# Kernel optimization log

Hardware: AMD Instinct MI355X
Metric: run time of the kernel (lower is better)

## Reference

```python
import jax, jax.numpy as jnp
import numpy as np
import math

B, N, F_IN, F_OUT = 8, 2048, 128, 128


def _uniform(key, shape, stdv):
    return jax.random.uniform(key, shape, dtype=jnp.float32, minval=-stdv, maxval=stdv)


def setup_inputs() -> dict:
    key = jax.random.key(0)
    k_x, k_a, k_w, k_att, k_bw, k_ba = jax.random.split(key, 6)
    X = jax.random.normal(k_x, (B, N, F_IN), dtype=jnp.float32)
    # dense 0/1 adjacency, as consumed by torch.bmm(A, ...)
    A = jax.random.randint(k_a, (B, N, N), 0, 2).astype(jnp.float32)
    stdv_W = 1.0 / math.sqrt(F_OUT)        # W.size(1) == n_fea_out
    stdv_a = 1.0 / math.sqrt(2 * F_OUT)    # a.size(1) == 2*n_fea_out
    W = _uniform(k_w, (F_IN, F_OUT), stdv_W)
    a = _uniform(k_att, (1, 2 * F_OUT), stdv_a)
    bias_W = _uniform(k_bw, (F_OUT,), stdv_W)
    bias_a = _uniform(k_ba, (N,), stdv_a)
    return {"X": X, "A": A, "W": W, "a": a, "bias_a": bias_a, "bias_W": bias_W}


def reference(X, A, W, a, bias_a, bias_W):
    # XW: [B, N, F_out]
    XW = jnp.einsum('bnf,fo->bno', X, W)
    f = W.shape[1]
    # Original materializes Z[b,i,j] = concat(XW[b,j], XW[b,i]) then dots with a.
    # This is separable: Z1[b,i,j] = a[:f]@XW[b,j] + a[f:]@XW[b,i] + bias_a[j]
    a_j = a[0, :f]   # multiplies XW[b, j]
    a_i = a[0, f:]   # multiplies XW[b, i]
    s_j = jnp.einsum('bnf,f->bn', XW, a_j)  # [B, N]
    s_i = jnp.einsum('bnf,f->bn', XW, a_i)  # [B, N]
    Z1 = s_i[:, :, None] + s_j[:, None, :] + bias_a[None, None, :]  # [B, N, N]
    den = jnp.exp(Z1)
    num = jnp.einsum('bik,bkj->bij', A, den)  # torch.bmm(A, denominator)
    # where numerator == 0 the torch code leaves att uninitialized; use 0 deterministically
    nz = num != 0
    att = jnp.where(nz, den / jnp.where(nz, num, 1.0), 0.0)
    buf = jnp.einsum('bij,bjf->bif', att, XW)
    H = jnp.einsum('bij,bjf->bif', A, buf) + bias_W
    return H
```

## Files before the change

kernel.cpp:

```cpp
#include <hip/hip_runtime.h>

#define BB 8
#define NN 2048
#define FF 128


__global__ __launch_bounds__(128) void k0_wai(const float* __restrict__ W,
                                              const float* __restrict__ a,
                                              float* __restrict__ w_ai) {
    int c = threadIdx.x;
    float s = 0.f;
#pragma unroll 8
    for (int f = 0; f < FF; ++f) s += W[c * FF + f] * a[FF + f];
    w_ai[c] = s;
}

__global__ __launch_bounds__(256) void k1_p_xsum(const float* __restrict__ X,
                                                 const float* __restrict__ w_ai,
                                                 float* __restrict__ p,
                                                 float* __restrict__ xsum) {
    __shared__ float xls[FF];
    int gr0 = blockIdx.x * 32;
    int b = gr0 >> 11;
    int lane = threadIdx.x & 63;
    int wave = threadIdx.x >> 6;
    int half = lane >> 5;
    int l32 = lane & 31;

    if (threadIdx.x < FF) xls[threadIdx.x] = 0.f;
    __syncthreads();

    float4 wv = ((const float4*)w_ai)[l32];
    float4 cs = make_float4(0.f, 0.f, 0.f, 0.f);
    const float4* X4 = (const float4*)(X + (size_t)gr0 * FF);

#pragma unroll
    for (int it = 0; it < 4; ++it) {
        int rloc = wave * 8 + it * 2 + half;
        float4 xv = X4[(size_t)rloc * 32 + l32];
        cs.x += xv.x; cs.y += xv.y; cs.z += xv.z; cs.w += xv.w;
        float s = xv.x * wv.x + xv.y * wv.y + xv.z * wv.z + xv.w * wv.w;
#pragma unroll
        for (int off = 16; off; off >>= 1) s += __shfl_xor(s, off, 64);
        if (l32 == 0) p[(size_t)gr0 + rloc] = expf(s);
    }

    atomicAdd(&xls[l32 * 4 + 0], cs.x);
    atomicAdd(&xls[l32 * 4 + 1], cs.y);
    atomicAdd(&xls[l32 * 4 + 2], cs.z);
    atomicAdd(&xls[l32 * 4 + 3], cs.w);
    __syncthreads();
    if (threadIdx.x < FF) atomicAdd(&xsum[b * FF + threadIdx.x], xls[threadIdx.x]);
}

__global__ __launch_bounds__(128) void k2_S(const float* __restrict__ W,
                                            const float* __restrict__ xsum,
                                            float* __restrict__ S) {
    int b = blockIdx.x;
    int f = threadIdx.x;
    float s = 0.f;
#pragma unroll 8
    for (int c = 0; c < FF; ++c) s += xsum[b * FF + c] * W[c * FF + f];
    S[b * FF + f] = s;
}

__global__ __launch_bounds__(256) void k3_r(const float* __restrict__ A,
                                            const float* __restrict__ p,
                                            float* __restrict__ r,
                                            unsigned long long* __restrict__ pk) {
    __shared__ float p_lds[NN];
    int row0 = blockIdx.x * 8;
    int b = row0 >> 11;

    const float4* p4 = (const float4*)(p + (size_t)b * NN);
    float4* pl4 = (float4*)p_lds;
    pl4[threadIdx.x]       = p4[threadIdx.x];
    pl4[threadIdx.x + 256] = p4[threadIdx.x + 256];
    __syncthreads();

    int lane = threadIdx.x & 63;
    int wave = threadIdx.x >> 6;
    int rowA = row0 + wave * 2;
    int rowB = rowA + 1;
    const float4* Aa = (const float4*)(A + (size_t)rowA * NN);
    const float4* Ab = (const float4*)(A + (size_t)rowB * NN);

    int c = lane & 3;
    float accA = 0.f, accB = 0.f;
#pragma unroll
    for (int it = 0; it < 8; ++it) {
        float4 pv = pl4[it * 64 + lane];
        float4 va = Aa[it * 64 + lane];
        float4 vb = Ab[it * 64 + lane];
        accA += va.x * pv.x + va.y * pv.y + va.z * pv.z + va.w * pv.w;
        accB += vb.x * pv.x + vb.y * pv.y + vb.z * pv.z + vb.w * pv.w;

        unsigned long long a0 = __ballot(va.x != 0.f);
        unsigned long long a1 = __ballot(va.y != 0.f);
        unsigned long long a2 = __ballot(va.z != 0.f);
        unsigned long long a3 = __ballot(va.w != 0.f);
        unsigned long long b0 = __ballot(vb.x != 0.f);
        unsigned long long b1 = __ballot(vb.y != 0.f);
        unsigned long long b2 = __ballot(vb.z != 0.f);
        unsigned long long b3 = __ballot(vb.w != 0.f);
        if (lane < 8) {
            unsigned long long alo = (c & 1) ? a1 : a0;
            unsigned long long ahi = (c & 1) ? a3 : a2;
            unsigned long long am  = (c & 2) ? ahi : alo;
            unsigned long long blo = (c & 1) ? b1 : b0;
            unsigned long long bhi = (c & 1) ? b3 : b2;
            unsigned long long bm  = (c & 2) ? bhi : blo;
            int row = (lane < 4) ? rowA : rowB;
            unsigned long long m = (lane < 4) ? am : bm;
            pk[(size_t)row * 32 + it * 4 + c] = m;
        }
    }
#pragma unroll
    for (int off = 32; off; off >>= 1) {
        accA += __shfl_xor(accA, off, 64);
        accB += __shfl_xor(accB, off, 64);
    }

    if (lane == 0) {
        r[rowA] = (accA != 0.f) ? (p_lds[rowA & (NN - 1)] / accA) : 0.f;
        r[rowB] = (accB != 0.f) ? (p_lds[rowB & (NN - 1)] / accB) : 0.f;
    }
}

__global__ __launch_bounds__(256) void k4_H(const unsigned long long* __restrict__ pk,
                                            const float* __restrict__ rr,
                                            const float* __restrict__ S,
                                            const float* __restrict__ bias_W,
                                            float* __restrict__ Hout) {
    __shared__ float r_lds[NN];
    __shared__ float s_lds[FF];
    __shared__ float bw_lds[FF];
    int row0 = blockIdx.x * 8;
    int b = row0 >> 11;

    const float4* r4 = (const float4*)(rr + (size_t)b * NN);
    float4* rl4 = (float4*)r_lds;
    rl4[threadIdx.x]       = r4[threadIdx.x];
    rl4[threadIdx.x + 256] = r4[threadIdx.x + 256];
    if (threadIdx.x < FF) {
        s_lds[threadIdx.x]  = S[b * FF + threadIdx.x];
        bw_lds[threadIdx.x] = bias_W[threadIdx.x];
    }
    __syncthreads();

    int lane = threadIdx.x & 63;
    int wave = threadIdx.x >> 6;
    int rowA = row0 + wave * 2;
    int rowB = rowA + 1;

    unsigned long long w =
        pk[(size_t)(lane < 32 ? rowA : rowB) * 32 + (lane & 31)];

    float accA = 0.f, accB = 0.f;
#pragma unroll
    for (int it = 0; it < 8; ++it) {
        float4 rv = rl4[it * 64 + lane];
        unsigned long long mA0 = __shfl(w, it * 4 + 0, 64);
        unsigned long long mA1 = __shfl(w, it * 4 + 1, 64);
        unsigned long long mA2 = __shfl(w, it * 4 + 2, 64);
        unsigned long long mA3 = __shfl(w, it * 4 + 3, 64);
        unsigned long long mB0 = __shfl(w, 32 + it * 4 + 0, 64);
        unsigned long long mB1 = __shfl(w, 32 + it * 4 + 1, 64);
        unsigned long long mB2 = __shfl(w, 32 + it * 4 + 2, 64);
        unsigned long long mB3 = __shfl(w, 32 + it * 4 + 3, 64);
        if ((mA0 >> lane) & 1ull) accA += rv.x;
        if ((mA1 >> lane) & 1ull) accA += rv.y;
        if ((mA2 >> lane) & 1ull) accA += rv.z;
        if ((mA3 >> lane) & 1ull) accA += rv.w;
        if ((mB0 >> lane) & 1ull) accB += rv.x;
        if ((mB1 >> lane) & 1ull) accB += rv.y;
        if ((mB2 >> lane) & 1ull) accB += rv.z;
        if ((mB3 >> lane) & 1ull) accB += rv.w;
    }
#pragma unroll
    for (int off = 32; off; off >>= 1) {
        accA += __shfl_xor(accA, off, 64);
        accB += __shfl_xor(accB, off, 64);
    }

    float2 sv = ((const float2*)s_lds)[lane];
    float2 bv = ((const float2*)bw_lds)[lane];
    float2* H2 = (float2*)Hout;
    float2 ha, hb;
    ha.x = accA * sv.x + bv.x;  ha.y = accA * sv.y + bv.y;
    hb.x = accB * sv.x + bv.x;  hb.y = accB * sv.y + bv.y;
    H2[(size_t)rowA * 64 + lane] = ha;
    H2[(size_t)rowB * 64 + lane] = hb;
}

extern "C" void kernel_launch(void* const* d_in, const int* in_sizes, int n_in,
                              void* d_out, int out_size, void* d_ws, size_t ws_size,
                              hipStream_t stream) {
    const float* X      = (const float*)d_in[0];
    const float* A      = (const float*)d_in[1];
    const float* W      = (const float*)d_in[2];
    const float* a      = (const float*)d_in[3];
    const float* bias_W = (const float*)d_in[5];
    float* out = (float*)d_out;

    float* ws   = (float*)d_ws;
    float* w_ai = ws;
    float* xsum = ws + 128;
    float* S    = ws + 1152;
    float* p    = ws + 2176;
    float* r    = ws + 18560;
    unsigned long long* pk = (unsigned long long*)(ws + 34944);

    hipMemsetAsync(xsum, 0, BB * FF * sizeof(float), stream);

    k0_wai<<<1, 128, 0, stream>>>(W, a, w_ai);
    k1_p_xsum<<<(BB * NN) / 32, 256, 0, stream>>>(X, w_ai, p, xsum);
    k2_S<<<BB, 128, 0, stream>>>(W, xsum, S);
    k3_r<<<(BB * NN) / 8, 256, 0, stream>>>(A, p, r, pk);
    k4_H<<<(BB * NN) / 8, 256, 0, stream>>>(pk, r, S, bias_W, out);
}
```

Measured before the change: 240.7 us.

## Fold tiny prologue kernels into main kernels and drop memset

Computes W·a_i redundantly in every k1 block instead of a separate launch. k1 now writes per-block partial column sums instead of using global atomics, and an extra block 0 in k3 reduces them and computes S. This removes two kernel launches and a memset, trading them for redundant small matvecs per block and one serial extra block inside k3. k3 is dominated by the A read, so the added block should matter little.

After: 236.2 us. About the same (-1.9%).

```diff
diff --git a/kernel.cpp b/kernel.cpp
--- a/kernel.cpp
+++ b/kernel.cpp
@@ -5,32 +5,30 @@
 #define FF 128
 
 
-__global__ __launch_bounds__(128) void k0_wai(const float* __restrict__ W,
-                                              const float* __restrict__ a,
-                                              float* __restrict__ w_ai) {
-    int c = threadIdx.x;
-    float s = 0.f;
+__global__ __launch_bounds__(256) void k1_p_xsum(const float* __restrict__ X,
+                                                 const float* __restrict__ W,
+                                                 const float* __restrict__ a,
+                                                 float* __restrict__ p,
+                                                 float* __restrict__ xpart) {
+    __shared__ float wls[FF];
+    __shared__ float xls[FF];
+    int t = threadIdx.x;
+    if (t < FF) {
+        float s = 0.f;
 #pragma unroll 8
-    for (int f = 0; f < FF; ++f) s += W[c * FF + f] * a[FF + f];
-    w_ai[c] = s;
-}
-
-__global__ __launch_bounds__(256) void k1_p_xsum(const float* __restrict__ X,
-                                                 const float* __restrict__ w_ai,
-                                                 float* __restrict__ p,
-                                                 float* __restrict__ xsum) {
-    __shared__ float xls[FF];
+        for (int f = 0; f < FF; ++f) s += W[t * FF + f] * a[FF + f];
+        wls[t] = s;
+        xls[t] = 0.f;
+    }
+    __syncthreads();
+
     int gr0 = blockIdx.x * 32;
-    int b = gr0 >> 11;
-    int lane = threadIdx.x & 63;
-    int wave = threadIdx.x >> 6;
+    int lane = t & 63;
+    int wave = t >> 6;
     int half = lane >> 5;
     int l32 = lane & 31;
 
-    if (threadIdx.x < FF) xls[threadIdx.x] = 0.f;
-    __syncthreads();
-
-    float4 wv = ((const float4*)w_ai)[l32];
+    float4 wv = ((const float4*)wls)[l32];
     float4 cs = make_float4(0.f, 0.f, 0.f, 0.f);
     const float4* X4 = (const float4*)(X + (size_t)gr0 * FF);
 
@@ -50,36 +48,52 @@
     atomicAdd(&xls[l32 * 4 + 2], cs.z);
     atomicAdd(&xls[l32 * 4 + 3], cs.w);
     __syncthreads();
-    if (threadIdx.x < FF) atomicAdd(&xsum[b * FF + threadIdx.x], xls[threadIdx.x]);
-}
-
-__global__ __launch_bounds__(128) void k2_S(const float* __restrict__ W,
-                                            const float* __restrict__ xsum,
-                                            float* __restrict__ S) {
-    int b = blockIdx.x;
-    int f = threadIdx.x;
-    float s = 0.f;
-#pragma unroll 8
-    for (int c = 0; c < FF; ++c) s += xsum[b * FF + c] * W[c * FF + f];
-    S[b * FF + f] = s;
+    if (t < FF) xpart[blockIdx.x * FF + t] = xls[t];
 }
 
 __global__ __launch_bounds__(256) void k3_r(const float* __restrict__ A,
+                                            const float* __restrict__ W,
+                                            const float* __restrict__ xpart,
                                             const float* __restrict__ p,
                                             float* __restrict__ r,
+                                            float* __restrict__ S,
                                             unsigned long long* __restrict__ pk) {
     __shared__ float p_lds[NN];
-    int row0 = blockIdx.x * 8;
+    int t = threadIdx.x;
+
+    if (blockIdx.x == 0) {
+#pragma unroll
+        for (int k = 0; k < 4; ++k) {
+            int o = t + 256 * k;
+            int b = o >> 7, f = o & 127;
+            float s = 0.f;
+            for (int j = 0; j < 64; ++j) s += xpart[(b * 64 + j) * FF + f];
+            p_lds[o] = s;
+        }
+        __syncthreads();
+#pragma unroll
+        for (int k = 0; k < 4; ++k) {
+            int o = t + 256 * k;
+            int b = o >> 7, f = o & 127;
+            float s = 0.f;
+#pragma unroll 8
+            for (int c = 0; c < FF; ++c) s += p_lds[b * FF + c] * W[c * FF + f];
+            S[o] = s;
+        }
+        return;
+    }
+
+    int row0 = (blockIdx.x - 1) * 8;
     int b = row0 >> 11;
 
     const float4* p4 = (const float4*)(p + (size_t)b * NN);
     float4* pl4 = (float4*)p_lds;
-    pl4[threadIdx.x]       = p4[threadIdx.x];
-    pl4[threadIdx.x + 256] = p4[threadIdx.x + 256];
-    __syncthreads();
-
-    int lane = threadIdx.x & 63;
-    int wave = threadIdx.x >> 6;
+    pl4[t]       = p4[t];
+    pl4[t + 256] = p4[t + 256];
+    __syncthreads();
+
+    int lane = t & 63;
+    int wave = t >> 6;
     int rowA = row0 + wave * 2;
     int rowB = rowA + 1;
     const float4* Aa = (const float4*)(A + (size_t)rowA * NN);
@@ -203,19 +217,14 @@
     const float* bias_W = (const float*)d_in[5];
     float* out = (float*)d_out;
 
-    float* ws   = (float*)d_ws;
-    float* w_ai = ws;
-    float* xsum = ws + 128;
-    float* S    = ws + 1152;
-    float* p    = ws + 2176;
-    float* r    = ws + 18560;
-    unsigned long long* pk = (unsigned long long*)(ws + 34944);
-
-    hipMemsetAsync(xsum, 0, BB * FF * sizeof(float), stream);
-
-    k0_wai<<<1, 128, 0, stream>>>(W, a, w_ai);
-    k1_p_xsum<<<(BB * NN) / 32, 256, 0, stream>>>(X, w_ai, p, xsum);
-    k2_S<<<BB, 128, 0, stream>>>(W, xsum, S);
-    k3_r<<<(BB * NN) / 8, 256, 0, stream>>>(A, p, r, pk);
+    float* ws    = (float*)d_ws;
+    float* xpart = ws;
+    float* S     = ws + 65536;
+    float* p     = ws + 66560;
+    float* r     = ws + 82944;
+    unsigned long long* pk = (unsigned long long*)(ws + 99328);
+
+    k1_p_xsum<<<(BB * NN) / 32, 256, 0, stream>>>(X, W, a, p, xpart);
+    k3_r<<<(BB * NN) / 8 + 1, 256, 0, stream>>>(A, W, xpart, p, r, S, pk);
     k4_H<<<(BB * NN) / 8, 256, 0, stream>>>(pk, r, S, bias_W, out);
 }
```
